# Optimization experiments

Measured on AMD Instinct MI355X. Metric: run time of the kernel, lower is better.

## Reference

```python
import jax, jax.numpy as jnp
import numpy as np

B, E, T, MAX_LEN = 8192, 1024, 64, 20
EPS = 1e-08


def setup_inputs() -> dict:
    key = jax.random.key(0)
    ks = jax.random.split(key, 8)
    s = 1.0 / np.sqrt(E)
    return {
        "h_t": jax.random.normal(ks[0], (B, E), dtype=jnp.float32),
        "testing": 0,
        "emb": jax.random.normal(ks[1], (T, E), dtype=jnp.float32),
        "W_ih": jax.random.uniform(ks[2], (4 * E, E), minval=-s, maxval=s, dtype=jnp.float32),
        "W_hh": jax.random.uniform(ks[3], (4 * E, E), minval=-s, maxval=s, dtype=jnp.float32),
        "b_ih": jax.random.uniform(ks[4], (4 * E,), minval=-s, maxval=s, dtype=jnp.float32),
        "b_hh": jax.random.uniform(ks[5], (4 * E,), minval=-s, maxval=s, dtype=jnp.float32),
        "W1": jax.random.uniform(ks[6], (T, E), minval=-s, maxval=s, dtype=jnp.float32),
        "b1": jax.random.uniform(ks[7], (T,), minval=-s, maxval=s, dtype=jnp.float32),
    }


def reference(h_t, testing, emb, W_ih, W_hh, b_ih, b_hh, W1, b1):
    batch = h_t.shape[0]
    c0 = jnp.zeros_like(h_t)
    tok0 = jnp.zeros((batch,), dtype=jnp.int32)

    def step(carry, key_i):
        h, c, last = carry
        x = emb[last]  # [B, E] embedding lookup
        gates = x @ W_ih.T + b_ih + h @ W_hh.T + b_hh  # [B, 4E]
        i_g, f_g, g_g, o_g = jnp.split(gates, 4, axis=1)  # PyTorch LSTMCell gate order i,f,g,o
        i_g = jax.nn.sigmoid(i_g)
        f_g = jax.nn.sigmoid(f_g)
        g_g = jnp.tanh(g_g)
        o_g = jax.nn.sigmoid(o_g)
        c = f_g * c + i_g * g_g
        h = o_g * jnp.tanh(c)
        logits = h @ W1.T + b1  # [B, T]
        probs = jax.nn.softmax(logits, axis=1)
        greedy = jnp.argmax(probs, axis=1)
        if testing:
            a = greedy
            log_g = jnp.zeros((batch,), dtype=probs.dtype)
        else:
            a = jax.random.categorical(key_i, logits, axis=1)  # multinomial(probs, 1)
            log_g = jnp.log(jnp.take_along_axis(probs, a[:, None], axis=1))[:, 0]
        matches = (greedy == a).sum()
        p = probs + EPS
        ent = -(p * jnp.log(p)).sum()
        return (h, c, a), (log_g, a, ent, matches)

    keys = jax.random.split(jax.random.key(42), MAX_LEN)
    (_, _, _), (log_gs, toks, ents, matches) = jax.lax.scan(step, (h_t, c0, tok0), keys)
    utterance = toks.T  # [B, MAX_LEN]
    entropy = ents.sum()
    matches_argmax_count = matches.sum()
    stochastic_draws_count = batch * MAX_LEN
    return (log_gs, utterance, entropy, matches_argmax_count, stochastic_draws_count)
```

## Files before the change

kernel.cpp:

```cpp
#include <hip/hip_runtime.h>
#include <hip/hip_bf16.h>
#include <stdint.h>
#include <math.h>

#define BB   8192
#define EE   1024
#define GG   4096
#define TTK  64
#define LLEN 20

#define PRNG_PARTITIONABLE 1

typedef __attribute__((ext_vector_type(8)))  __bf16 bf16x8;
typedef __attribute__((ext_vector_type(4)))  __bf16 bf16x4;
typedef __attribute__((ext_vector_type(16))) float  f32x16;

__host__ __device__ __forceinline__ void tf2x32(unsigned k0, unsigned k1,
                                                unsigned x0, unsigned x1,
                                                unsigned& o0, unsigned& o1) {
  unsigned ks2 = k0 ^ k1 ^ 0x1BD11BDAu;
#define TFR(r) { x0 += x1; x1 = (x1 << (r)) | (x1 >> (32 - (r))); x1 ^= x0; }
  x0 += k0; x1 += k1;
  TFR(13) TFR(15) TFR(26) TFR(6)  x0 += k1;  x1 += ks2 + 1u;
  TFR(17) TFR(29) TFR(16) TFR(24) x0 += ks2; x1 += k0 + 2u;
  TFR(13) TFR(15) TFR(26) TFR(6)  x0 += k0;  x1 += k1 + 3u;
  TFR(17) TFR(29) TFR(16) TFR(24) x0 += k1;  x1 += ks2 + 4u;
  TFR(13) TFR(15) TFR(26) TFR(6)  x0 += ks2; x1 += k0 + 5u;
#undef TFR
  o0 = x0; o1 = x1;
}

__device__ __forceinline__ float wave_max64(float v) {
#pragma unroll
  for (int o = 32; o > 0; o >>= 1) v = fmaxf(v, __shfl_xor(v, o));
  return v;
}
__device__ __forceinline__ float wave_sum64(float v) {
#pragma unroll
  for (int o = 32; o > 0; o >>= 1) v += __shfl_xor(v, o);
  return v;
}
__device__ __forceinline__ void wave_argmax64(float v, int i, float& rv, int& ri) {
  rv = v; ri = i;
#pragma unroll
  for (int o = 32; o > 0; o >>= 1) {
    float ov = __shfl_xor(rv, o);
    int   oi = __shfl_xor(ri, o);
    if (ov > rv || (ov == rv && oi < ri)) { rv = ov; ri = oi; }
  }
}

__device__ __forceinline__ void gl16(const __bf16* g, __bf16* l) {
  __builtin_amdgcn_global_load_lds(
      (const __attribute__((address_space(1))) void*)g,
      (__attribute__((address_space(3))) void*)l, 16, 0, 0);
}

__global__ void split3_kernel(const float* __restrict__ in, __bf16* __restrict__ s0,
                              __bf16* __restrict__ s1, __bf16* __restrict__ s2, int n) {
  int i = blockIdx.x * blockDim.x + threadIdx.x;
  int stride = gridDim.x * blockDim.x;
  for (; i < n; i += stride) {
    float x = in[i];
    __bf16 a = (__bf16)x; float r1 = x - (float)a;
    __bf16 b = (__bf16)r1; float r2 = r1 - (float)b;
    s0[i] = a; s1[i] = b; s2[i] = (__bf16)r2;
  }
}

__global__ __launch_bounds__(256)
void embw_kernel(const float* __restrict__ emb, const float* __restrict__ Wih,
                 const float* __restrict__ bih, float* __restrict__ embW,
                 float* __restrict__ ent_acc, int* __restrict__ match_acc) {
  if (blockIdx.x == 0 && threadIdx.x == 0) { *ent_acc = 0.0f; *match_acc = 0; }
  __shared__ float hsm[64][36];
  __shared__ float wsm[64][65];
  const int j0 = blockIdx.x * 32;
  const int tid = threadIdx.x;
  const int wv = tid >> 6, lane = tid & 63;
  float acc[8];
#pragma unroll
  for (int r = 0; r < 8; r++) acc[r] = 0.0f;

  for (int k0 = 0; k0 < EE; k0 += 64) {
    {
      int row = tid >> 3, kb = (tid & 7) * 8;
      const float4* p = reinterpret_cast<const float4*>(Wih + (size_t)(j0 + row) * EE + k0 + kb);
      float4 v0 = p[0], v1 = p[1];
      hsm[kb + 0][row] = v0.x; hsm[kb + 1][row] = v0.y; hsm[kb + 2][row] = v0.z; hsm[kb + 3][row] = v0.w;
      hsm[kb + 4][row] = v1.x; hsm[kb + 5][row] = v1.y; hsm[kb + 6][row] = v1.z; hsm[kb + 7][row] = v1.w;
      int tr = tid >> 2, kc = (tid & 3) * 16;
      const float4* q = reinterpret_cast<const float4*>(emb + (size_t)tr * EE + k0 + kc);
#pragma unroll
      for (int i = 0; i < 4; i++) {
        float4 a = q[i];
        wsm[tr][kc + i * 4 + 0] = a.x; wsm[tr][kc + i * 4 + 1] = a.y;
        wsm[tr][kc + i * 4 + 2] = a.z; wsm[tr][kc + i * 4 + 3] = a.w;
      }
    }
    __syncthreads();
#pragma unroll
    for (int k = 0; k < 64; k++) {
      float w0 = wsm[lane][k];
      float4 va = *reinterpret_cast<const float4*>(&hsm[k][wv * 8]);
      float4 vb = *reinterpret_cast<const float4*>(&hsm[k][wv * 8 + 4]);
      acc[0] = fmaf(va.x, w0, acc[0]); acc[1] = fmaf(va.y, w0, acc[1]);
      acc[2] = fmaf(va.z, w0, acc[2]); acc[3] = fmaf(va.w, w0, acc[3]);
      acc[4] = fmaf(vb.x, w0, acc[4]); acc[5] = fmaf(vb.y, w0, acc[5]);
      acc[6] = fmaf(vb.z, w0, acc[6]); acc[7] = fmaf(vb.w, w0, acc[7]);
    }
    __syncthreads();
  }
#pragma unroll
  for (int r = 0; r < 8; r++) {
    int j = j0 + wv * 8 + r;
    embW[(size_t)lane * GG + j] = __fadd_rn(acc[r], bih[j]);
  }
}

#define AST   104
#define BUFE  39936
__global__ __launch_bounds__(256, 2)
void lstm_mfma_kernel(const __bf16* __restrict__ hA0, const __bf16* __restrict__ hA1,
                      const __bf16* __restrict__ hA2,
                      __bf16* __restrict__ hN0, __bf16* __restrict__ hN1,
                      __bf16* __restrict__ hN2,
                      float* __restrict__ cbuf,
                      const __bf16* __restrict__ w0s, const __bf16* __restrict__ w1s,
                      const __bf16* __restrict__ w2s,
                      const float* __restrict__ embW, const float* __restrict__ bhh,
                      const int* __restrict__ tok, int step) {
  __shared__ __bf16 lds[BUFE];
  unsigned bid = blockIdx.x;
  unsigned xcd = bid & 7, j = bid >> 3;
  unsigned xm = xcd >> 1, xn = xcd & 1;
  const int m = (int)(xm * 8 + (j & 7));
  const int n = (int)(xn * 16 + (j >> 3));
  const int row0 = m * 256, e0 = n * 32;
  const int tid = threadIdx.x;
  const int w = tid >> 6, l = tid & 63;

  f32x16 acc[2][4];
#pragma unroll
  for (int rt = 0; rt < 2; rt++)
#pragma unroll
    for (int ct = 0; ct < 4; ct++)
#pragma unroll
      for (int q = 0; q < 16; q++) acc[rt][ct][q] = 0.0f;

  const __bf16* aSrcP[13];
  const __bf16* bSrcP[7];
  const int nB = (w < 2) ? 7 : 6;
#pragma unroll
  for (int i = 0; i < 13; i++) {
    int slot = (w * 13 + i) * 64 + l;
    int row = slot / 13, chk = slot - row * 13;
    const __bf16* base;
    size_t off;
    if (chk < 12) {
      int s = chk >> 2, q = chk & 3;
      base = (s == 0) ? hA0 : (s == 1) ? hA1 : hA2;
      off = (size_t)(row0 + row) * EE + q * 8;
    } else { base = hA0; off = 0; }
    aSrcP[i] = base + off;
  }
#pragma unroll
  for (int i = 0; i < 7; i++) {
    if (i < nB) {
      int ib = w + i * 4;
      int slot = ib * 64 + l;
      int c = slot / 13, chk = slot - c * 13;
      const __bf16* base;
      size_t off;
      if (chk < 12) {
        int s = chk >> 2, q = chk & 3;
        int jj = (c >> 5) * 1024 + e0 + (c & 31);
        base = (s == 0) ? w0s : (s == 1) ? w1s : w2s;
        off = (size_t)jj * EE + q * 8;
      } else { base = w0s; off = 0; }
      bSrcP[i] = base + off;
    }
  }
  const int aDstOff = w * 13 * 512;
  const int bDstOff = 26624 + w * 512;

#define STAGE(KE) do {                                                   \
    _Pragma("unroll")                                                    \
    for (int i_ = 0; i_ < 13; i_++)                                      \
      gl16(aSrcP[i_] + (KE), lds + aDstOff + i_ * 512);                  \
    _Pragma("unroll")                                                    \
    for (int i_ = 0; i_ < 7; i_++)                                       \
      if (i_ < nB) gl16(bSrcP[i_] + (KE), lds + bDstOff + i_ * 2048);    \
  } while (0)

  const __bf16* aB = lds + (w * 64 + (l & 31)) * AST + (l >> 5) * 8;
  const __bf16* bB = lds + (256 + (l & 31)) * AST + (l >> 5) * 8;

  for (int kt = 0; kt < 32; ++kt) {
    STAGE(kt * 32);
    asm volatile("s_waitcnt vmcnt(0)" ::: "memory");
    __builtin_amdgcn_s_barrier();
    __builtin_amdgcn_s_setprio(1);
#pragma unroll
    for (int kh = 0; kh < 2; kh++) {
      bf16x8 a[2][3];
#pragma unroll
      for (int rt = 0; rt < 2; rt++)
#pragma unroll
        for (int s = 0; s < 3; s++)
          a[rt][s] = *(const bf16x8*)(aB + rt * 32 * AST + s * 32 + kh * 16);
#pragma unroll
      for (int ct = 0; ct < 4; ct++) {
        bf16x8 b0 = *(const bf16x8*)(bB + ct * 32 * AST + 0  + kh * 16);
        bf16x8 b1 = *(const bf16x8*)(bB + ct * 32 * AST + 32 + kh * 16);
        bf16x8 b2 = *(const bf16x8*)(bB + ct * 32 * AST + 64 + kh * 16);
#pragma unroll
        for (int rt = 0; rt < 2; rt++) {
          f32x16 t = acc[rt][ct];
          t = __builtin_amdgcn_mfma_f32_32x32x16_bf16(a[rt][2], b0, t, 0, 0, 0);
          t = __builtin_amdgcn_mfma_f32_32x32x16_bf16(a[rt][0], b2, t, 0, 0, 0);
          t = __builtin_amdgcn_mfma_f32_32x32x16_bf16(a[rt][1], b1, t, 0, 0, 0);
          t = __builtin_amdgcn_mfma_f32_32x32x16_bf16(a[rt][1], b0, t, 0, 0, 0);
          t = __builtin_amdgcn_mfma_f32_32x32x16_bf16(a[rt][0], b1, t, 0, 0, 0);
          t = __builtin_amdgcn_mfma_f32_32x32x16_bf16(a[rt][0], b0, t, 0, 0, 0);
          acc[rt][ct] = t;
        }
      }
    }
    __builtin_amdgcn_s_setprio(0);
    asm volatile("s_waitcnt lgkmcnt(0)" ::: "memory");
    __builtin_amdgcn_s_barrier();
  }
#undef STAGE

  float* eC = ((float*)lds) + w * 2112;
  float* eH = eC + 1056;
  const int e_l = l & 31, half = l >> 5;
  float bh4[4];
#pragma unroll
  for (int g = 0; g < 4; g++) bh4[g] = bhh[g * 1024 + e0 + e_l];

#pragma unroll
  for (int rt = 0; rt < 2; rt++) {
    const int rowbase = row0 + w * 64 + rt * 32;
    {
      int r = l >> 3, ch = l & 7;
#pragma unroll
      for (int q = 0; q < 4; q++) {
        float4 cv;
        if (step == 0) cv = make_float4(0.f, 0.f, 0.f, 0.f);
        else cv = *(const float4*)(cbuf + (size_t)(rowbase + r + q * 8) * EE + e0 + ch * 4);
        *(float4*)(eC + (r + q * 8) * 33 + ch * 4) = cv;
      }
    }
    __syncthreads();
#pragma unroll
    for (int i = 0; i < 16; i++) {
      int rl = (i & 3) + 8 * (i >> 2) + 4 * half;
      int b = rowbase + rl;
      int tk = (step == 0) ? 0 : tok[b];
      const float* er = embW + (size_t)tk * GG;
      float g0 = __fadd_rn(__fadd_rn(er[0 * 1024 + e0 + e_l], acc[rt][0][i]), bh4[0]);
      float g1 = __fadd_rn(__fadd_rn(er[1 * 1024 + e0 + e_l], acc[rt][1][i]), bh4[1]);
      float g2 = __fadd_rn(__fadd_rn(er[2 * 1024 + e0 + e_l], acc[rt][2][i]), bh4[2]);
      float g3 = __fadd_rn(__fadd_rn(er[3 * 1024 + e0 + e_l], acc[rt][3][i]), bh4[3]);
      float ig = 1.0f / (1.0f + expf(-g0));
      float fg = 1.0f / (1.0f + expf(-g1));
      float gg = tanhf(g2);
      float og = 1.0f / (1.0f + expf(-g3));
      float co = eC[rl * 33 + e_l];
      float cn = __fadd_rn(__fmul_rn(fg, co), __fmul_rn(ig, gg));
      float hn = __fmul_rn(og, tanhf(cn));
      eC[rl * 33 + e_l] = cn;
      eH[rl * 33 + e_l] = hn;
    }
    __syncthreads();
    {
      int r = l >> 3, ch = l & 7;
#pragma unroll
      for (int q = 0; q < 4; q++) {
        int rr2 = r + q * 8;
        size_t gb = (size_t)(rowbase + rr2) * EE + e0 + ch * 4;
        *(float4*)(cbuf + gb) = *(const float4*)(eC + rr2 * 33 + ch * 4);
        float4 hv = *(const float4*)(eH + rr2 * 33 + ch * 4);
        float hf[4] = {hv.x, hv.y, hv.z, hv.w};
        bf16x4 o0, o1, o2;
#pragma unroll
        for (int jj = 0; jj < 4; jj++) {
          __bf16 a = (__bf16)hf[jj]; float r1 = hf[jj] - (float)a;
          __bf16 b = (__bf16)r1;     float r2 = r1 - (float)b;
          o0[jj] = a; o1[jj] = b; o2[jj] = (__bf16)r2;
        }
        *(bf16x4*)(hN0 + gb) = o0;
        *(bf16x4*)(hN1 + gb) = o1;
        *(bf16x4*)(hN2 + gb) = o2;
      }
    }
    __syncthreads();
  }
}

__global__ __launch_bounds__(256, 4)
void lstm_step_kernel(const float* __restrict__ hin, float* __restrict__ hout,
                      float* __restrict__ cbuf, const float* __restrict__ Whh,
                      const float* __restrict__ embW, const float* __restrict__ bhh,
                      const int* __restrict__ tok, int step) {
  __shared__ float hs[32][132];
  __shared__ float ws[32][132];
  const int row0 = blockIdx.x * 128;
  const int e0 = blockIdx.y * 32;
  const int tid = threadIdx.x;
  const int tx = tid & 15, ty = tid >> 4;
  float acc[8][4][2];
#pragma unroll
  for (int r = 0; r < 8; r++)
#pragma unroll
    for (int g = 0; g < 4; g++) { acc[r][g][0] = 0.0f; acc[r][g][1] = 0.0f; }

  const int lr = tid >> 3, lk = (tid & 7) * 4;
  for (int k0 = 0; k0 < EE; k0 += 32) {
#pragma unroll
    for (int rr = 0; rr < 4; rr++) {
      int row = lr + rr * 32;
      float4 v = *reinterpret_cast<const float4*>(hin + (size_t)(row0 + row) * EE + k0 + lk);
      hs[lk + 0][row] = v.x; hs[lk + 1][row] = v.y; hs[lk + 2][row] = v.z; hs[lk + 3][row] = v.w;
      int cg = row;
      int j = (cg >> 5) * 1024 + e0 + (cg & 31);
      float4 u = *reinterpret_cast<const float4*>(Whh + (size_t)j * EE + k0 + lk);
      ws[lk + 0][cg] = u.x; ws[lk + 1][cg] = u.y; ws[lk + 2][cg] = u.z; ws[lk + 3][cg] = u.w;
    }
    __syncthreads();
#pragma unroll
    for (int k = 0; k < 32; k++) {
      float4 va = *reinterpret_cast<const float4*>(&hs[k][ty * 8]);
      float4 vb = *reinterpret_cast<const float4*>(&hs[k][ty * 8 + 4]);
      float a0[8] = {va.x, va.y, va.z, va.w, vb.x, vb.y, vb.z, vb.w};
      float wvv[4][2];
#pragma unroll
      for (int g = 0; g < 4; g++) {
        float2 f2 = *reinterpret_cast<const float2*>(&ws[k][g * 32 + tx * 2]);
        wvv[g][0] = f2.x; wvv[g][1] = f2.y;
      }
#pragma unroll
      for (int r = 0; r < 8; r++)
#pragma unroll
        for (int g = 0; g < 4; g++) {
          acc[r][g][0] = fmaf(a0[r], wvv[g][0], acc[r][g][0]);
          acc[r][g][1] = fmaf(a0[r], wvv[g][1], acc[r][g][1]);
        }
    }
    __syncthreads();
  }
#pragma unroll
  for (int r = 0; r < 8; r++) {
    int b = row0 + ty * 8 + r;
    int tk = (step == 0) ? 0 : tok[b];
    const float* er = embW + (size_t)tk * GG;
#pragma unroll
    for (int x = 0; x < 2; x++) {
      int e = e0 + tx * 2 + x;
      float gate[4];
#pragma unroll
      for (int g = 0; g < 4; g++) {
        int j = g * 1024 + e;
        gate[g] = __fadd_rn(__fadd_rn(er[j], acc[r][g][x]), bhh[j]);
      }
      float ig = 1.0f / (1.0f + expf(-gate[0]));
      float fg = 1.0f / (1.0f + expf(-gate[1]));
      float gg = tanhf(gate[2]);
      float og = 1.0f / (1.0f + expf(-gate[3]));
      size_t idx = (size_t)b * EE + e;
      float cn;
      if (step == 0) cn = __fadd_rn(0.0f, __fmul_rn(ig, gg));
      else           cn = __fadd_rn(__fmul_rn(fg, cbuf[idx]), __fmul_rn(ig, gg));
      cbuf[idx] = cn;
      hout[idx] = __fmul_rn(og, tanhf(cn));
    }
  }
}

template <int HS>
__global__ __launch_bounds__(256)
void sample_kernel_t(const float* __restrict__ hf,
                     const __bf16* __restrict__ h0s, const __bf16* __restrict__ h1s,
                     const __bf16* __restrict__ h2s,
                     const float* __restrict__ W1, const float* __restrict__ b1,
                     int* __restrict__ tok, float* __restrict__ out,
                     float* __restrict__ ent_acc, int* __restrict__ match_acc,
                     int step, unsigned key0, unsigned key1) {
  __shared__ float hsm[64][36];
  __shared__ float wsm[64][65];
  __shared__ float entLds[4];
  __shared__ int   mLds[4];
  const int row0 = blockIdx.x * 32;
  const int tid = threadIdx.x;
  const int wv = tid >> 6, lane = tid & 63;
  float acc[8];
#pragma unroll
  for (int r = 0; r < 8; r++) acc[r] = 0.0f;

  for (int k0 = 0; k0 < EE; k0 += 64) {
    {
      int row = tid >> 3, kb = (tid & 7) * 8;
      if (HS) {
        size_t g = (size_t)(row0 + row) * EE + k0 + kb;
        bf16x8 u0 = *(const bf16x8*)(h0s + g);
        bf16x8 u1 = *(const bf16x8*)(h1s + g);
        bf16x8 u2 = *(const bf16x8*)(h2s + g);
#pragma unroll
        for (int j = 0; j < 8; j++)
          hsm[kb + j][row] = __fadd_rn(__fadd_rn((float)u0[j], (float)u1[j]), (float)u2[j]);
      } else {
        const float4* p = reinterpret_cast<const float4*>(hf + (size_t)(row0 + row) * EE + k0 + kb);
        float4 v0 = p[0], v1 = p[1];
        hsm[kb + 0][row] = v0.x; hsm[kb + 1][row] = v0.y; hsm[kb + 2][row] = v0.z; hsm[kb + 3][row] = v0.w;
        hsm[kb + 4][row] = v1.x; hsm[kb + 5][row] = v1.y; hsm[kb + 6][row] = v1.z; hsm[kb + 7][row] = v1.w;
      }
      int tr = tid >> 2, kc = (tid & 3) * 16;
      const float4* q = reinterpret_cast<const float4*>(W1 + (size_t)tr * EE + k0 + kc);
#pragma unroll
      for (int i = 0; i < 4; i++) {
        float4 a = q[i];
        wsm[tr][kc + i * 4 + 0] = a.x; wsm[tr][kc + i * 4 + 1] = a.y;
        wsm[tr][kc + i * 4 + 2] = a.z; wsm[tr][kc + i * 4 + 3] = a.w;
      }
    }
    __syncthreads();
#pragma unroll
    for (int k = 0; k < 64; k++) {
      float w0 = wsm[lane][k];
      float4 va = *reinterpret_cast<const float4*>(&hsm[k][wv * 8]);
      float4 vb = *reinterpret_cast<const float4*>(&hsm[k][wv * 8 + 4]);
      acc[0] = fmaf(va.x, w0, acc[0]); acc[1] = fmaf(va.y, w0, acc[1]);
      acc[2] = fmaf(va.z, w0, acc[2]); acc[3] = fmaf(va.w, w0, acc[3]);
      acc[4] = fmaf(vb.x, w0, acc[4]); acc[5] = fmaf(vb.y, w0, acc[5]);
      acc[6] = fmaf(vb.z, w0, acc[6]); acc[7] = fmaf(vb.w, w0, acc[7]);
    }
    __syncthreads();
  }

  const float b1v = b1[lane];
  float entLane = 0.0f;
  int mcnt = 0;
#pragma unroll 1
  for (int r = 0; r < 8; r++) {
    int b = row0 + wv * 8 + r;
    float lg = __fadd_rn(acc[r], b1v);
    float mx = wave_max64(lg);
    float e = expf(lg - mx);
    float s = wave_sum64(e);
    float p = e / s;
    float gv; int gi; wave_argmax64(p, lane, gv, gi);
    unsigned nidx = (unsigned)(b * 64 + lane);
    unsigned o0, o1, bits;
#if PRNG_PARTITIONABLE
    tf2x32(key0, key1, 0u, nidx, o0, o1);
    bits = o0 ^ o1;
#else
    const unsigned HALF = (BB * TTK) / 2;
    if (nidx < HALF) { tf2x32(key0, key1, nidx, nidx + HALF, o0, o1); bits = o0; }
    else             { tf2x32(key0, key1, nidx - HALF, nidx, o0, o1); bits = o1; }
#endif
    float f = __uint_as_float((bits >> 9) | 0x3f800000u) - 1.0f;
    float u = fmaxf(1.17549435e-38f, f);
    float gum = -logf(-logf(u));
    float z = __fadd_rn(gum, lg);
    float zv; int zi; wave_argmax64(z, lane, zv, zi);
    float pa = __shfl(p, zi);
    if (lane == 0) {
      out[step * BB + b] = logf(pa);
      out[BB * LLEN + b * LLEN + step] = (float)zi;
      tok[b] = zi;
      if (gi == zi) mcnt++;
    }
    float pp = p + 1e-8f;
    entLane += pp * logf(pp);
  }
  float esum = wave_sum64(entLane);
  if (lane == 0) { entLds[wv] = esum; mLds[wv] = mcnt; }
  __syncthreads();
  if (tid == 0) {
    atomicAdd(ent_acc, entLds[0] + entLds[1] + entLds[2] + entLds[3]);
    atomicAdd(match_acc, mLds[0] + mLds[1] + mLds[2] + mLds[3]);
  }
}

__global__ void finalize_kernel(float* __restrict__ out,
                                const float* __restrict__ ent_acc,
                                const int* __restrict__ match_acc) {
  if (threadIdx.x == 0) {
    out[2 * BB * LLEN + 0] = -(*ent_acc);
    out[2 * BB * LLEN + 1] = (float)(*match_acc);
    out[2 * BB * LLEN + 2] = (float)(BB * LLEN);
  }
}

extern "C" void kernel_launch(void* const* d_in, const int* in_sizes, int n_in,
                              void* d_out, int out_size, void* d_ws, size_t ws_size,
                              hipStream_t stream) {
  const float* h_t = (const float*)d_in[0];
  const float* emb = (const float*)d_in[2];
  const float* Wih = (const float*)d_in[3];
  const float* Whh = (const float*)d_in[4];
  const float* bih = (const float*)d_in[5];
  const float* bhh = (const float*)d_in[6];
  const float* W1  = (const float*)d_in[7];
  const float* b1  = (const float*)d_in[8];
  float* out = (float*)d_out;

  unsigned k0s[LLEN], k1s[LLEN];
#if PRNG_PARTITIONABLE
  for (int s = 0; s < LLEN; s++) {
    unsigned a, b2; tf2x32(0u, 42u, 0u, (unsigned)s, a, b2);
    k0s[s] = a; k1s[s] = b2;
  }
#else
  {
    unsigned bitsArr[40];
    for (int j = 0; j < 20; j++) {
      unsigned a, b2; tf2x32(0u, 42u, (unsigned)j, (unsigned)(j + 20), a, b2);
      bitsArr[j] = a; bitsArr[20 + j] = b2;
    }
    for (int s = 0; s < LLEN; s++) { k0s[s] = bitsArr[2 * s]; k1s[s] = bitsArr[2 * s + 1]; }
  }
#endif

  const size_t NE = (size_t)BB * EE;
  const size_t WN = (size_t)GG * EE;
  const size_t NEED = NE * 4 + 6 * NE * 2 + 3 * WN * 2 + (size_t)TTK * GG * 4 + BB * 4 + 64;

  if (ws_size >= NEED) {
    char* p = (char*)d_ws;
    float*  cbuf = (float*)p;            p += NE * 4;
    __bf16* hA0  = (__bf16*)p;           p += NE * 2;
    __bf16* hA1  = (__bf16*)p;           p += NE * 2;
    __bf16* hA2  = (__bf16*)p;           p += NE * 2;
    __bf16* hB0  = (__bf16*)p;           p += NE * 2;
    __bf16* hB1  = (__bf16*)p;           p += NE * 2;
    __bf16* hB2  = (__bf16*)p;           p += NE * 2;
    __bf16* w0   = (__bf16*)p;           p += WN * 2;
    __bf16* w1   = (__bf16*)p;           p += WN * 2;
    __bf16* w2   = (__bf16*)p;           p += WN * 2;
    float*  embW = (float*)p;            p += (size_t)TTK * GG * 4;
    int*    tok  = (int*)p;              p += BB * 4;
    float*  ent_acc = (float*)p;
    int*    match_acc = (int*)(p + 4);

    hipLaunchKernelGGL(split3_kernel, dim3(512), dim3(256), 0, stream,
                       h_t, hA0, hA1, hA2, (int)NE);
    hipLaunchKernelGGL(split3_kernel, dim3(512), dim3(256), 0, stream,
                       Whh, w0, w1, w2, (int)WN);
    hipLaunchKernelGGL(embw_kernel, dim3(128), dim3(256), 0, stream,
                       emb, Wih, bih, embW, ent_acc, match_acc);
    for (int s = 0; s < LLEN; s++) {
      const __bf16 *r0 = (s & 1) ? hB0 : hA0, *r1 = (s & 1) ? hB1 : hA1, *r2 = (s & 1) ? hB2 : hA2;
      __bf16 *n0 = (s & 1) ? hA0 : hB0, *n1 = (s & 1) ? hA1 : hB1, *n2 = (s & 1) ? hA2 : hB2;
      hipLaunchKernelGGL(lstm_mfma_kernel, dim3(1024), dim3(256), 0, stream,
                         r0, r1, r2, n0, n1, n2, cbuf, w0, w1, w2, embW, bhh, tok, s);
      hipLaunchKernelGGL((sample_kernel_t<1>), dim3(256), dim3(256), 0, stream,
                         (const float*)nullptr, n0, n1, n2, W1, b1, tok, out,
                         ent_acc, match_acc, s, k0s[s], k1s[s]);
    }
    hipLaunchKernelGGL(finalize_kernel, dim3(1), dim3(64), 0, stream,
                       out, ent_acc, match_acc);
  } else {
    float* ws = (float*)d_ws;
    float* h0   = ws;
    float* h1   = ws + NE;
    float* cbuf = ws + 2 * NE;
    float* embW = ws + 3 * NE;
    int*   tok  = (int*)(ws + 3 * NE + (size_t)TTK * GG);
    float* ent_acc = (float*)(tok + BB);
    int*   match_acc = (int*)(ent_acc + 1);

    hipLaunchKernelGGL(embw_kernel, dim3(128), dim3(256), 0, stream,
                       emb, Wih, bih, embW, ent_acc, match_acc);
    for (int s = 0; s < LLEN; s++) {
      const float* hin = (s == 0) ? h_t : ((s & 1) ? h0 : h1);
      float* hout = (s & 1) ? h1 : h0;
      hipLaunchKernelGGL(lstm_step_kernel, dim3(64, 32), dim3(256), 0, stream,
                         hin, hout, cbuf, Whh, embW, bhh, tok, s);
      hipLaunchKernelGGL((sample_kernel_t<0>), dim3(256), dim3(256), 0, stream,
                         hout, (const __bf16*)nullptr, (const __bf16*)nullptr,
                         (const __bf16*)nullptr, W1, b1, tok, out,
                         ent_acc, match_acc, s, k0s[s], k1s[s]);
    }
    hipLaunchKernelGGL(finalize_kernel, dim3(1), dim3(64), 0, stream,
                       out, ent_acc, match_acc);
  }
}
```

Measured before the change: 8.791 ms.

## Double-buffer LDS tiles with K=16 steps and XOR-swizzled layout in LSTM MFMA kernel

```diff
diff --git a/kernel.cpp b/kernel.cpp
--- a/kernel.cpp
+++ b/kernel.cpp
@@ -118,8 +118,8 @@
   }
 }
 
-#define AST   104
-#define BUFE  39936
+#define AST16  48
+#define BUFE16 18432
 __global__ __launch_bounds__(256, 2)
 void lstm_mfma_kernel(const __bf16* __restrict__ hA0, const __bf16* __restrict__ hA1,
                       const __bf16* __restrict__ hA2,
@@ -130,12 +130,12 @@
                       const __bf16* __restrict__ w2s,
                       const float* __restrict__ embW, const float* __restrict__ bhh,
                       const int* __restrict__ tok, int step) {
-  __shared__ __bf16 lds[BUFE];
+  __shared__ __bf16 lds[2 * BUFE16];
   unsigned bid = blockIdx.x;
-  unsigned xcd = bid & 7, j = bid >> 3;
+  unsigned xcd = bid & 7, j0b = bid >> 3;
   unsigned xm = xcd >> 1, xn = xcd & 1;
-  const int m = (int)(xm * 8 + (j & 7));
-  const int n = (int)(xn * 16 + (j >> 3));
+  const int m = (int)(xm * 8 + (j0b & 7));
+  const int n = (int)(xn * 16 + (j0b >> 3));
   const int row0 = m * 256, e0 = n * 32;
   const int tid = threadIdx.x;
   const int w = tid >> 6, l = tid & 63;
@@ -148,87 +148,77 @@
 #pragma unroll
       for (int q = 0; q < 16; q++) acc[rt][ct][q] = 0.0f;
 
-  const __bf16* aSrcP[13];
-  const __bf16* bSrcP[7];
-  const int nB = (w < 2) ? 7 : 6;
-#pragma unroll
-  for (int i = 0; i < 13; i++) {
-    int slot = (w * 13 + i) * 64 + l;
-    int row = slot / 13, chk = slot - row * 13;
-    const __bf16* base;
-    size_t off;
-    if (chk < 12) {
-      int s = chk >> 2, q = chk & 3;
+  const __bf16* src[9];
+#pragma unroll
+  for (int i = 0; i < 9; i++) {
+    int c = i * 256 + tid;
+    int row = c / 6, tp = c - row * 6;
+    int t = tp ^ ((row >> 2) & 1);
+    int s = t >> 1, hf = t & 1;
+    const __bf16* base; size_t off;
+    if (row < 256) {
       base = (s == 0) ? hA0 : (s == 1) ? hA1 : hA2;
-      off = (size_t)(row0 + row) * EE + q * 8;
-    } else { base = hA0; off = 0; }
-    aSrcP[i] = base + off;
-  }
-#pragma unroll
-  for (int i = 0; i < 7; i++) {
-    if (i < nB) {
-      int ib = w + i * 4;
-      int slot = ib * 64 + l;
-      int c = slot / 13, chk = slot - c * 13;
-      const __bf16* base;
-      size_t off;
-      if (chk < 12) {
-        int s = chk >> 2, q = chk & 3;
-        int jj = (c >> 5) * 1024 + e0 + (c & 31);
-        base = (s == 0) ? w0s : (s == 1) ? w1s : w2s;
-        off = (size_t)jj * EE + q * 8;
-      } else { base = w0s; off = 0; }
-      bSrcP[i] = base + off;
-    }
-  }
-  const int aDstOff = w * 13 * 512;
-  const int bDstOff = 26624 + w * 512;
-
-#define STAGE(KE) do {                                                   \
+      off = (size_t)(row0 + row) * EE + hf * 8;
+    } else {
+      int c2 = row - 256;
+      int jj = (c2 >> 5) * 1024 + e0 + (c2 & 31);
+      base = (s == 0) ? w0s : (s == 1) ? w1s : w2s;
+      off = (size_t)jj * EE + hf * 8;
+    }
+    src[i] = base + off;
+  }
+  const int dstT = tid * 8;
+
+#define STAGE(BUF, KE) do {                                              \
     _Pragma("unroll")                                                    \
-    for (int i_ = 0; i_ < 13; i_++)                                      \
-      gl16(aSrcP[i_] + (KE), lds + aDstOff + i_ * 512);                  \
-    _Pragma("unroll")                                                    \
-    for (int i_ = 0; i_ < 7; i_++)                                       \
-      if (i_ < nB) gl16(bSrcP[i_] + (KE), lds + bDstOff + i_ * 2048);    \
+    for (int i_ = 0; i_ < 9; i_++)                                       \
+      gl16(src[i_] + (KE), lds + (BUF) + i_ * 2048 + dstT);              \
   } while (0)
 
-  const __bf16* aB = lds + (w * 64 + (l & 31)) * AST + (l >> 5) * 8;
-  const __bf16* bB = lds + (256 + (l & 31)) * AST + (l >> 5) * 8;
-
-  for (int kt = 0; kt < 32; ++kt) {
-    STAGE(kt * 32);
-    asm volatile("s_waitcnt vmcnt(0)" ::: "memory");
-    __builtin_amdgcn_s_barrier();
+  const int li = l & 31, hf = l >> 5, sb = (l >> 2) & 1;
+  int tps[3];
+#pragma unroll
+  for (int s = 0; s < 3; s++) tps[s] = ((s * 2 + hf) ^ sb) * 8;
+  int aBase[2], bBase[4];
+#pragma unroll
+  for (int rt = 0; rt < 2; rt++) aBase[rt] = (w * 64 + rt * 32 + li) * AST16;
+#pragma unroll
+  for (int ct = 0; ct < 4; ct++) bBase[ct] = (256 + ct * 32 + li) * AST16;
+
+  STAGE(0, 0);
+  asm volatile("s_waitcnt vmcnt(0)" ::: "memory");
+  __builtin_amdgcn_s_barrier();
+
+  for (int kt = 0; kt < 64; ++kt) {
+    const int cur = (kt & 1) * BUFE16;
+    if (kt < 63) STAGE(cur ^ BUFE16, (kt + 1) * 16);
+    const __bf16* base = lds + cur;
     __builtin_amdgcn_s_setprio(1);
-#pragma unroll
-    for (int kh = 0; kh < 2; kh++) {
-      bf16x8 a[2][3];
-#pragma unroll
-      for (int rt = 0; rt < 2; rt++)
-#pragma unroll
-        for (int s = 0; s < 3; s++)
-          a[rt][s] = *(const bf16x8*)(aB + rt * 32 * AST + s * 32 + kh * 16);
-#pragma unroll
-      for (int ct = 0; ct < 4; ct++) {
-        bf16x8 b0 = *(const bf16x8*)(bB + ct * 32 * AST + 0  + kh * 16);
-        bf16x8 b1 = *(const bf16x8*)(bB + ct * 32 * AST + 32 + kh * 16);
-        bf16x8 b2 = *(const bf16x8*)(bB + ct * 32 * AST + 64 + kh * 16);
-#pragma unroll
-        for (int rt = 0; rt < 2; rt++) {
-          f32x16 t = acc[rt][ct];
-          t = __builtin_amdgcn_mfma_f32_32x32x16_bf16(a[rt][2], b0, t, 0, 0, 0);
-          t = __builtin_amdgcn_mfma_f32_32x32x16_bf16(a[rt][0], b2, t, 0, 0, 0);
-          t = __builtin_amdgcn_mfma_f32_32x32x16_bf16(a[rt][1], b1, t, 0, 0, 0);
-          t = __builtin_amdgcn_mfma_f32_32x32x16_bf16(a[rt][1], b0, t, 0, 0, 0);
-          t = __builtin_amdgcn_mfma_f32_32x32x16_bf16(a[rt][0], b1, t, 0, 0, 0);
-          t = __builtin_amdgcn_mfma_f32_32x32x16_bf16(a[rt][0], b0, t, 0, 0, 0);
-          acc[rt][ct] = t;
-        }
+    bf16x8 a[2][3];
+#pragma unroll
+    for (int rt = 0; rt < 2; rt++)
+#pragma unroll
+      for (int s = 0; s < 3; s++)
+        a[rt][s] = *(const bf16x8*)(base + aBase[rt] + tps[s]);
+#pragma unroll
+    for (int ct = 0; ct < 4; ct++) {
+      bf16x8 b0 = *(const bf16x8*)(base + bBase[ct] + tps[0]);
+      bf16x8 b1 = *(const bf16x8*)(base + bBase[ct] + tps[1]);
+      bf16x8 b2 = *(const bf16x8*)(base + bBase[ct] + tps[2]);
+#pragma unroll
+      for (int rt = 0; rt < 2; rt++) {
+        f32x16 t = acc[rt][ct];
+        t = __builtin_amdgcn_mfma_f32_32x32x16_bf16(a[rt][2], b0, t, 0, 0, 0);
+        t = __builtin_amdgcn_mfma_f32_32x32x16_bf16(a[rt][0], b2, t, 0, 0, 0);
+        t = __builtin_amdgcn_mfma_f32_32x32x16_bf16(a[rt][1], b1, t, 0, 0, 0);
+        t = __builtin_amdgcn_mfma_f32_32x32x16_bf16(a[rt][1], b0, t, 0, 0, 0);
+        t = __builtin_amdgcn_mfma_f32_32x32x16_bf16(a[rt][0], b1, t, 0, 0, 0);
+        t = __builtin_amdgcn_mfma_f32_32x32x16_bf16(a[rt][0], b0, t, 0, 0, 0);
+        acc[rt][ct] = t;
       }
     }
     __builtin_amdgcn_s_setprio(0);
-    asm volatile("s_waitcnt lgkmcnt(0)" ::: "memory");
+    asm volatile("s_waitcnt vmcnt(0) lgkmcnt(0)" ::: "memory");
     __builtin_amdgcn_s_barrier();
   }
 #undef STAGE
@@ -283,12 +273,12 @@
         size_t gb = (size_t)(rowbase + rr2) * EE + e0 + ch * 4;
         *(float4*)(cbuf + gb) = *(const float4*)(eC + rr2 * 33 + ch * 4);
         float4 hv = *(const float4*)(eH + rr2 * 33 + ch * 4);
-        float hf[4] = {hv.x, hv.y, hv.z, hv.w};
+        float hf2[4] = {hv.x, hv.y, hv.z, hv.w};
         bf16x4 o0, o1, o2;
 #pragma unroll
         for (int jj = 0; jj < 4; jj++) {
-          __bf16 a = (__bf16)hf[jj]; float r1 = hf[jj] - (float)a;
-          __bf16 b = (__bf16)r1;     float r2 = r1 - (float)b;
+          __bf16 a = (__bf16)hf2[jj]; float r1 = hf2[jj] - (float)a;
+          __bf16 b = (__bf16)r1;      float r2 = r1 - (float)b;
           o0[jj] = a; o1[jj] = b; o2[jj] = (__bf16)r2;
         }
         *(bf16x4*)(hN0 + gb) = o0;
```

New measurement: 9.635 ms. +9.6%, slower.
